# Optimization experiments

Hardware: AMD Instinct MI355X
Metric: run time of the kernel (lower is better)

The kernel has to match this reference:

```python
import jax, jax.numpy as jnp
import numpy as np

B, V = 256, 128000

def setup_inputs() -> dict:
    key = jax.random.key(0)
    k1, k2 = jax.random.split(key)
    logits = jax.random.normal(k1, (B, V), dtype=jnp.float32)
    temperatures = jax.random.uniform(k2, (B,), dtype=jnp.float32)
    return {"logits": logits, "temperatures": temperatures}

def reference(logits, temperatures):
    # temperature-scaled probs (float32), temp==0 treated as 1 for the divide
    logits_f = logits.astype(jnp.float32)
    safe_t = jnp.where(temperatures == 0, jnp.ones_like(temperatures), temperatures)
    scaled = logits_f / safe_t[:, None]                      # [B, V]
    probs = jax.nn.softmax(scaled, axis=-1)                  # [B, V] fp32
    # greedy tokens from the ORIGINAL logits (torch in-place div only touched the copy)
    greedy_tokens = jnp.argmax(logits_f, axis=-1)            # [B] int
    # multinomial sampling == Gumbel-max / categorical over scaled logits
    sample_key = jax.random.key(42)
    sampled_tokens = jax.random.categorical(sample_key, scaled, axis=-1)  # [B]
    tokens = jnp.where(temperatures == 0, greedy_tokens, sampled_tokens)
    return tokens, probs
```

## Files before the change

kernel.cpp:

```cpp
#include <hip/hip_runtime.h>
#include <cstdint>
#include <cmath>

#define B_ROWS 256
#define V_COLS 128000
#define CHUNKS 25
#define CHUNK_QUADS 1280
#define ATHREADS 256
#define AWAVES 4
#define QPT 5
#define ELEMS_PT 20
#define LN2F 0.69314718055994530942f

#define P_STRIDE 4
#define FIN_OFF (B_ROWS * CHUNKS * P_STRIDE)

__device__ __forceinline__ uint32_t rotl32(uint32_t x, uint32_t d) {
  return __builtin_amdgcn_alignbit(x, x, 32u - d);
}

__device__ __forceinline__ uint32_t threefry_xor(uint32_t x0, uint32_t x1) {
  const uint32_t k0 = 0u;
  const uint32_t k1 = 42u;
  const uint32_t k2 = 0x1BD11BDAu ^ k0 ^ k1;
  x0 += k0; x1 += k1;
#define TF_RND(r) { x0 += x1; x1 = rotl32(x1, (r)); x1 ^= x0; }
  TF_RND(13) TF_RND(15) TF_RND(26) TF_RND(6)
  x0 += k1; x1 += k2 + 1u;
  TF_RND(17) TF_RND(29) TF_RND(16) TF_RND(24)
  x0 += k2; x1 += k0 + 2u;
  TF_RND(13) TF_RND(15) TF_RND(26) TF_RND(6)
  x0 += k0; x1 += k1 + 3u;
  TF_RND(17) TF_RND(29) TF_RND(16) TF_RND(24)
  x0 += k1; x1 += k2 + 4u;
  TF_RND(13) TF_RND(15) TF_RND(26) TF_RND(6)
  x0 += k2; x1 += k0 + 5u;
#undef TF_RND
  return x0 ^ x1;
}

__device__ __forceinline__ float gumbel_l2(uint32_t bits) {
  uint32_t ub = (bits >> 9) | 0x3f800000u;
  float f = __uint_as_float(ub) - 1.0f;
  float u = fmaxf(f, 1.17549435e-38f);
  const float l1 = __log2f(u);
  const float nl = -LN2F * l1;
  return __log2f(nl);
}

__global__ __launch_bounds__(ATHREADS, 4) void partial_kernel(
    const float* __restrict__ logits,
    const float* __restrict__ temps,
    float* __restrict__ ws) {
  const uint32_t bx = blockIdx.x;
  const uint32_t b = bx / CHUNKS;
  const uint32_t chunk = bx - b * CHUNKS;
  const int tid = threadIdx.x;
  const float t = temps[b];
  const float inv_t = (t == 0.0f) ? 1.0f : (1.0f / t);
  const float* __restrict__ row = logits + (size_t)b * V_COLS;
  const int q0 = (int)chunk * CHUNK_QUADS + tid;

  float4 xq[QPT];
#pragma unroll
  for (int j = 0; j < QPT; ++j)
    xq[j] = reinterpret_cast<const float4*>(row)[q0 + j * ATHREADS];

  float sx[ELEMS_PT];
#pragma unroll
  for (int j = 0; j < QPT; ++j) {
    sx[4 * j + 0] = xq[j].x * inv_t;
    sx[4 * j + 1] = xq[j].y * inv_t;
    sx[4 * j + 2] = xq[j].z * inv_t;
    sx[4 * j + 3] = xq[j].w * inv_t;
  }

  float mthr = sx[0];
#pragma unroll
  for (int k = 1; k < ELEMS_PT; ++k) mthr = fmaxf(mthr, sx[k]);

  float s = 0.0f;
#pragma unroll
  for (int k = 0; k < ELEMS_PT; ++k) s += __expf(sx[k] - mthr);

  float av = -INFINITY; int ai = 0;
  const int v0 = q0 * 4;
  if (t != 0.0f) {
    const uint32_t cb = b * (uint32_t)V_COLS + (uint32_t)v0;
#pragma unroll
    for (int j = 0; j < QPT; ++j) {
#pragma unroll
      for (int k = 0; k < 4; ++k) {
        const float c = fmaf(-LN2F,
            gumbel_l2(threefry_xor(0u, cb + (uint32_t)(j * 1024 + k))),
            sx[4 * j + k]);
        const bool up = c > av;
        av = up ? c : av;
        ai = up ? (v0 + j * 1024 + k) : ai;
      }
    }
  } else {
#pragma unroll
    for (int j = 0; j < QPT; ++j) {
#pragma unroll
      for (int k = 0; k < 4; ++k) {
        const float x = sx[4 * j + k];
        const bool up = x > av;
        av = up ? x : av;
        ai = up ? (v0 + j * 1024 + k) : ai;
      }
    }
  }

  float m = mthr;
#pragma unroll
  for (int off = 32; off > 0; off >>= 1) {
    float ov = __shfl_xor(av, off);
    int   oi = __shfl_xor(ai, off);
    if (ov > av || (ov == av && oi < ai)) { av = ov; ai = oi; }
    float om = __shfl_xor(m, off);
    float os = __shfl_xor(s, off);
    float mn = fmaxf(m, om);
    s = fmaf(s, __expf(m - mn), os * __expf(om - mn));
    m = mn;
  }

  __shared__ float lds_av[AWAVES]; __shared__ int lds_ai[AWAVES];
  __shared__ float lds_m[AWAVES];  __shared__ float lds_s[AWAVES];
  const int wid = tid >> 6;
  if ((tid & 63) == 0) {
    lds_av[wid] = av; lds_ai[wid] = ai;
    lds_m[wid] = m;   lds_s[wid] = s;
  }
  __syncthreads();
  if (tid == 0) {
    float Av = lds_av[0]; int Ai = lds_ai[0];
    float M = lds_m[0];   float S = lds_s[0];
#pragma unroll
    for (int w = 1; w < AWAVES; ++w) {
      float ov = lds_av[w]; int oi = lds_ai[w];
      if (ov > Av || (ov == Av && oi < Ai)) { Av = ov; Ai = oi; }
      float om = lds_m[w]; float os = lds_s[w];
      float mn = fmaxf(M, om);
      S = fmaf(S, __expf(M - mn), os * __expf(om - mn));
      M = mn;
    }
    float* p = ws + (size_t)(b * CHUNKS + chunk) * P_STRIDE;
    p[0] = Av; p[1] = __int_as_float(Ai);
    p[2] = M;  p[3] = S;
  }
}

__global__ __launch_bounds__(B_ROWS) void finalize_kernel(
    const float* __restrict__ temps,
    float* __restrict__ ws,
    float* __restrict__ out) {
  const int r = threadIdx.x;
  const float* p = ws + (size_t)r * CHUNKS * P_STRIDE;
  float Av = -INFINITY; int Ai = 0;
  float M = -INFINITY;  float S = 0.0f;
#pragma unroll
  for (int c = 0; c < CHUNKS; ++c) {
    const float* q = p + c * P_STRIDE;
    float ov = q[0]; int oi = __float_as_int(q[1]);
    if (ov > Av) { Av = ov; Ai = oi; }
    float om = q[2]; float os = q[3];
    float mn = fmaxf(M, om);
    S = fmaf(S, __expf(M - mn), os * __expf(om - mn));
    M = mn;
  }
  out[r] = (float)Ai;
  ws[FIN_OFF + 2 * r]     = M;
  ws[FIN_OFF + 2 * r + 1] = 1.0f / S;
}

__global__ __launch_bounds__(ATHREADS, 4) void probs_kernel(
    const float* __restrict__ logits,
    const float* __restrict__ temps,
    const float* __restrict__ ws,
    float* __restrict__ out) {
  const uint32_t bx = blockIdx.x;
  const uint32_t b = bx / CHUNKS;
  const uint32_t chunk = bx - b * CHUNKS;
  const int tid = threadIdx.x;
  const float t = temps[b];
  const float inv_t = (t == 0.0f) ? 1.0f : (1.0f / t);
  const float M = ws[FIN_OFF + 2 * b];
  const float invS = ws[FIN_OFF + 2 * b + 1];
  const float* __restrict__ row = logits + (size_t)b * V_COLS;
  float* __restrict__ prow = out + B_ROWS + (size_t)b * V_COLS;
  const int q0 = (int)chunk * CHUNK_QUADS + tid;

#pragma unroll
  for (int j = 0; j < QPT; ++j) {
    const float4 x4 = reinterpret_cast<const float4*>(row)[q0 + j * ATHREADS];
    float4 p4;
    p4.x = __expf(fmaf(x4.x, inv_t, -M)) * invS;
    p4.y = __expf(fmaf(x4.y, inv_t, -M)) * invS;
    p4.z = __expf(fmaf(x4.z, inv_t, -M)) * invS;
    p4.w = __expf(fmaf(x4.w, inv_t, -M)) * invS;
    reinterpret_cast<float4*>(prow)[q0 + j * ATHREADS] = p4;
  }
}

extern "C" void kernel_launch(void* const* d_in, const int* in_sizes, int n_in,
                              void* d_out, int out_size, void* d_ws, size_t ws_size,
                              hipStream_t stream) {
  const float* logits = (const float*)d_in[0];
  const float* temps  = (const float*)d_in[1];
  float* out = (float*)d_out;
  float* ws  = (float*)d_ws;
  partial_kernel<<<B_ROWS * CHUNKS, ATHREADS, 0, stream>>>(logits, temps, ws);
  finalize_kernel<<<1, B_ROWS, 0, stream>>>(temps, ws, out);
  probs_kernel<<<B_ROWS * CHUNKS, ATHREADS, 0, stream>>>(logits, temps, ws, out);
}
```

Before: 119.6 us.

## Move Gumbel sampling from the reduction pass into the probs-writing pass

The threefry RNG and Gumbel argmax move out of the first pass, which now computes only max/sum and the greedy argmax, into the second pass that writes probabilities. The second pass reduces a per-chunk sampled argmax, and a new finalize kernel picks greedy or sampled tokens per row. The aim is to hide the ALU-heavy RNG work behind the store-bound probs pass, balancing compute and memory across the two passes. It adds a fourth launch and extra workspace traffic.

```diff
diff --git a/kernel.cpp b/kernel.cpp
--- a/kernel.cpp
+++ b/kernel.cpp
@@ -12,8 +12,9 @@
 #define ELEMS_PT 20
 #define LN2F 0.69314718055994530942f
 
-#define P_STRIDE 4
-#define FIN_OFF (B_ROWS * CHUNKS * P_STRIDE)
+#define G_STRIDE 4
+#define FIN_OFF (B_ROWS * CHUNKS * G_STRIDE)
+#define S_OFF (FIN_OFF + B_ROWS * 4)
 
 __device__ __forceinline__ uint32_t rotl32(uint32_t x, uint32_t d) {
   return __builtin_amdgcn_alignbit(x, x, 32u - d);
@@ -48,7 +49,7 @@
   return __log2f(nl);
 }
 
-__global__ __launch_bounds__(ATHREADS, 4) void partial_kernel(
+__global__ __launch_bounds__(ATHREADS, 4) void pass1_kernel(
     const float* __restrict__ logits,
     const float* __restrict__ temps,
     float* __restrict__ ws) {
@@ -78,37 +79,20 @@
   float mthr = sx[0];
 #pragma unroll
   for (int k = 1; k < ELEMS_PT; ++k) mthr = fmaxf(mthr, sx[k]);
-
   float s = 0.0f;
 #pragma unroll
   for (int k = 0; k < ELEMS_PT; ++k) s += __expf(sx[k] - mthr);
 
   float av = -INFINITY; int ai = 0;
   const int v0 = q0 * 4;
-  if (t != 0.0f) {
-    const uint32_t cb = b * (uint32_t)V_COLS + (uint32_t)v0;
-#pragma unroll
-    for (int j = 0; j < QPT; ++j) {
-#pragma unroll
-      for (int k = 0; k < 4; ++k) {
-        const float c = fmaf(-LN2F,
-            gumbel_l2(threefry_xor(0u, cb + (uint32_t)(j * 1024 + k))),
-            sx[4 * j + k]);
-        const bool up = c > av;
-        av = up ? c : av;
-        ai = up ? (v0 + j * 1024 + k) : ai;
-      }
-    }
-  } else {
-#pragma unroll
-    for (int j = 0; j < QPT; ++j) {
-#pragma unroll
-      for (int k = 0; k < 4; ++k) {
-        const float x = sx[4 * j + k];
-        const bool up = x > av;
-        av = up ? x : av;
-        ai = up ? (v0 + j * 1024 + k) : ai;
-      }
+#pragma unroll
+  for (int j = 0; j < QPT; ++j) {
+    const float xa[4] = {xq[j].x, xq[j].y, xq[j].z, xq[j].w};
+#pragma unroll
+    for (int k = 0; k < 4; ++k) {
+      const bool up = xa[k] > av;
+      av = up ? xa[k] : av;
+      ai = up ? (v0 + j * 1024 + k) : ai;
     }
   }
 
@@ -145,23 +129,21 @@
       S = fmaf(S, __expf(M - mn), os * __expf(om - mn));
       M = mn;
     }
-    float* p = ws + (size_t)(b * CHUNKS + chunk) * P_STRIDE;
+    float* p = ws + (size_t)(b * CHUNKS + chunk) * G_STRIDE;
     p[0] = Av; p[1] = __int_as_float(Ai);
     p[2] = M;  p[3] = S;
   }
 }
 
-__global__ __launch_bounds__(B_ROWS) void finalize_kernel(
-    const float* __restrict__ temps,
-    float* __restrict__ ws,
-    float* __restrict__ out) {
+__global__ __launch_bounds__(B_ROWS) void fin1_kernel(
+    float* __restrict__ ws) {
   const int r = threadIdx.x;
-  const float* p = ws + (size_t)r * CHUNKS * P_STRIDE;
+  const float* p = ws + (size_t)r * CHUNKS * G_STRIDE;
   float Av = -INFINITY; int Ai = 0;
   float M = -INFINITY;  float S = 0.0f;
 #pragma unroll
   for (int c = 0; c < CHUNKS; ++c) {
-    const float* q = p + c * P_STRIDE;
+    const float* q = p + c * G_STRIDE;
     float ov = q[0]; int oi = __float_as_int(q[1]);
     if (ov > Av) { Av = ov; Ai = oi; }
     float om = q[2]; float os = q[3];
@@ -169,15 +151,16 @@
     S = fmaf(S, __expf(M - mn), os * __expf(om - mn));
     M = mn;
   }
-  out[r] = (float)Ai;
-  ws[FIN_OFF + 2 * r]     = M;
-  ws[FIN_OFF + 2 * r + 1] = 1.0f / S;
-}
-
-__global__ __launch_bounds__(ATHREADS, 4) void probs_kernel(
+  float* f = ws + FIN_OFF + 4 * r;
+  f[0] = M;
+  f[1] = 1.0f / S;
+  f[2] = __int_as_float(Ai);
+}
+
+__global__ __launch_bounds__(ATHREADS, 4) void pass2_kernel(
     const float* __restrict__ logits,
     const float* __restrict__ temps,
-    const float* __restrict__ ws,
+    float* __restrict__ ws,
     float* __restrict__ out) {
   const uint32_t bx = blockIdx.x;
   const uint32_t b = bx / CHUNKS;
@@ -185,22 +168,89 @@
   const int tid = threadIdx.x;
   const float t = temps[b];
   const float inv_t = (t == 0.0f) ? 1.0f : (1.0f / t);
-  const float M = ws[FIN_OFF + 2 * b];
-  const float invS = ws[FIN_OFF + 2 * b + 1];
+  const float M = ws[FIN_OFF + 4 * b + 0];
+  const float invS = ws[FIN_OFF + 4 * b + 1];
   const float* __restrict__ row = logits + (size_t)b * V_COLS;
   float* __restrict__ prow = out + B_ROWS + (size_t)b * V_COLS;
   const int q0 = (int)chunk * CHUNK_QUADS + tid;
 
+  float4 xq[QPT];
+#pragma unroll
+  for (int j = 0; j < QPT; ++j)
+    xq[j] = reinterpret_cast<const float4*>(row)[q0 + j * ATHREADS];
+
 #pragma unroll
   for (int j = 0; j < QPT; ++j) {
-    const float4 x4 = reinterpret_cast<const float4*>(row)[q0 + j * ATHREADS];
     float4 p4;
-    p4.x = __expf(fmaf(x4.x, inv_t, -M)) * invS;
-    p4.y = __expf(fmaf(x4.y, inv_t, -M)) * invS;
-    p4.z = __expf(fmaf(x4.z, inv_t, -M)) * invS;
-    p4.w = __expf(fmaf(x4.w, inv_t, -M)) * invS;
+    p4.x = __expf(fmaf(xq[j].x, inv_t, -M)) * invS;
+    p4.y = __expf(fmaf(xq[j].y, inv_t, -M)) * invS;
+    p4.z = __expf(fmaf(xq[j].z, inv_t, -M)) * invS;
+    p4.w = __expf(fmaf(xq[j].w, inv_t, -M)) * invS;
     reinterpret_cast<float4*>(prow)[q0 + j * ATHREADS] = p4;
   }
+
+  float av = -INFINITY; int ai = 0;
+  if (t != 0.0f) {
+    const int v0 = q0 * 4;
+    const uint32_t cb = b * (uint32_t)V_COLS + (uint32_t)v0;
+#pragma unroll
+    for (int j = 0; j < QPT; ++j) {
+      const float xa[4] = {xq[j].x, xq[j].y, xq[j].z, xq[j].w};
+#pragma unroll
+      for (int k = 0; k < 4; ++k) {
+        const float sxv = xa[k] * inv_t;
+        const float c = fmaf(-LN2F,
+            gumbel_l2(threefry_xor(0u, cb + (uint32_t)(j * 1024 + k))), sxv);
+        const bool up = c > av;
+        av = up ? c : av;
+        ai = up ? (v0 + j * 1024 + k) : ai;
+      }
+    }
+  }
+
+#pragma unroll
+  for (int off = 32; off > 0; off >>= 1) {
+    float ov = __shfl_xor(av, off);
+    int   oi = __shfl_xor(ai, off);
+    if (ov > av || (ov == av && oi < ai)) { av = ov; ai = oi; }
+  }
+
+  __shared__ float lds_av[AWAVES]; __shared__ int lds_ai[AWAVES];
+  const int wid = tid >> 6;
+  if ((tid & 63) == 0) { lds_av[wid] = av; lds_ai[wid] = ai; }
+  __syncthreads();
+  if (tid == 0) {
+    float Av = lds_av[0]; int Ai = lds_ai[0];
+#pragma unroll
+    for (int w = 1; w < AWAVES; ++w) {
+      float ov = lds_av[w]; int oi = lds_ai[w];
+      if (ov > Av || (ov == Av && oi < Ai)) { Av = ov; Ai = oi; }
+    }
+    float* p = ws + S_OFF + (size_t)(b * CHUNKS + chunk) * 2;
+    p[0] = Av; p[1] = __int_as_float(Ai);
+  }
+}
+
+__global__ __launch_bounds__(B_ROWS) void fin2_kernel(
+    const float* __restrict__ temps,
+    const float* __restrict__ ws,
+    float* __restrict__ out) {
+  const int r = threadIdx.x;
+  const float t = temps[r];
+  int token;
+  if (t == 0.0f) {
+    token = __float_as_int(ws[FIN_OFF + 4 * r + 2]);
+  } else {
+    const float* p = ws + S_OFF + (size_t)r * CHUNKS * 2;
+    float Sv = -INFINITY; int Si = 0;
+#pragma unroll
+    for (int c = 0; c < CHUNKS; ++c) {
+      float ov = p[2 * c]; int oi = __float_as_int(p[2 * c + 1]);
+      if (ov > Sv) { Sv = ov; Si = oi; }
+    }
+    token = Si;
+  }
+  out[r] = (float)token;
 }
 
 extern "C" void kernel_launch(void* const* d_in, const int* in_sizes, int n_in,
@@ -210,7 +260,8 @@
   const float* temps  = (const float*)d_in[1];
   float* out = (float*)d_out;
   float* ws  = (float*)d_ws;
-  partial_kernel<<<B_ROWS * CHUNKS, ATHREADS, 0, stream>>>(logits, temps, ws);
-  finalize_kernel<<<1, B_ROWS, 0, stream>>>(temps, ws, out);
-  probs_kernel<<<B_ROWS * CHUNKS, ATHREADS, 0, stream>>>(logits, temps, ws, out);
-}
+  pass1_kernel<<<B_ROWS * CHUNKS, ATHREADS, 0, stream>>>(logits, temps, ws);
+  fin1_kernel<<<1, B_ROWS, 0, stream>>>(ws);
+  pass2_kernel<<<B_ROWS * CHUNKS, ATHREADS, 0, stream>>>(logits, temps, ws, out);
+  fin2_kernel<<<1, B_ROWS, 0, stream>>>(temps, ws, out);
+}
```

After: 110.5 us. -7.6%, faster.
